# Performance work log

Hardware: AMD Instinct MI355X
Metric: run time of the kernel (lower is better)

Reference implementation:

```python
import jax, jax.numpy as jnp
import numpy as np

B, S = 64, 1024
D_INPUT, D_POLAR, N_LAYERS, KAN, N_CLASSES = 256, 256, 8, 32, 1000
PI = float(np.pi)
EPS = 1e-8


def _gelu(v):
    return jax.nn.gelu(v, approximate=False)  # torch nn.GELU default = exact erf


def setup_inputs() -> dict:
    key = jax.random.key(0)
    ks = jax.random.split(key, 16)

    def rn(k, shape, fan_in):
        return jax.random.normal(k, shape, jnp.float32) / np.sqrt(fan_in)

    return {
        "x": jax.random.normal(ks[0], (B, S, D_INPUT), jnp.float32),
        "embed_w": rn(ks[1], (D_INPUT, 2 * D_POLAR), D_INPUT),
        "embed_b": jnp.zeros((2 * D_POLAR,), jnp.float32),
        "mag_w1": rn(ks[2], (N_LAYERS, 1, KAN), 1),
        "mag_b1": jnp.zeros((N_LAYERS, KAN), jnp.float32),
        "mag_w2": rn(ks[3], (N_LAYERS, KAN, 1), KAN),
        "mag_b2": jnp.zeros((N_LAYERS, 1), jnp.float32),
        "ph_w1": rn(ks[4], (N_LAYERS, 2, KAN), 2),
        "ph_b1": jnp.zeros((N_LAYERS, KAN), jnp.float32),
        "ph_w2": rn(ks[5], (N_LAYERS, KAN, 2), KAN),
        "ph_b2": jnp.zeros((N_LAYERS, 2), jnp.float32),
        "cls_w1": rn(ks[6], (D_POLAR, KAN), D_POLAR),
        "cls_b1": jnp.zeros((KAN,), jnp.float32),
        "cls_w2": rn(ks[7], (KAN, N_CLASSES), KAN),
        "cls_b2": jnp.zeros((N_CLASSES,), jnp.float32),
    }


def _forward(x, embed_w, embed_b, mag_w1, mag_b1, mag_w2, mag_b2,
             ph_w1, ph_b1, ph_w2, ph_b2, cls_w1, cls_b1, cls_w2, cls_b2):
    h = x @ embed_w + embed_b                      # [B,S,2D]
    r = jnp.abs(h[..., :D_POLAR]) + 0.1            # [B,S,D]
    theta = h[..., D_POLAR:] * PI                  # [B,S,D]
    for i in range(N_LAYERS):
        xc = r * jnp.cos(theta)
        yc = r * jnp.sin(theta)
        xm = xc.mean(axis=1, keepdims=True)        # [B,1,D]
        ym = yc.mean(axis=1, keepdims=True)
        r_agg = jnp.sqrt(xm * xm + ym * ym + EPS)
        th_agg = jnp.arctan2(ym, xm)
        # magnitude MLP (1 -> 32 -> 1) in log space, per channel
        log_r = jnp.log(r_agg + EPS)[..., None]    # [B,1,D,1]
        lr = _gelu(log_r @ mag_w1[i] + mag_b1[i]) @ mag_w2[i] + mag_b2[i]
        r_trans = jnp.exp(lr[..., 0])              # [B,1,D]
        # phase MLP (2 -> 32 -> 2) on (sin, cos)
        pin = jnp.stack([jnp.sin(th_agg), jnp.cos(th_agg)], axis=-1)  # [B,1,D,2]
        pout = _gelu(pin @ ph_w1[i] + ph_b1[i]) @ ph_w2[i] + ph_b2[i]
        norm = jnp.sqrt(pout[..., 0] ** 2 + pout[..., 1] ** 2 + EPS)
        th_trans = jnp.arctan2(pout[..., 0] / norm, pout[..., 1] / norm)
        x_out = xc + r_trans * jnp.cos(th_trans)
        y_out = yc + r_trans * jnp.sin(th_trans)
        r = jnp.sqrt(x_out * x_out + y_out * y_out + EPS)
        theta = jnp.arctan2(y_out, x_out)
    pooled = r.mean(axis=1)                        # [B,D]
    return _gelu(pooled @ cls_w1 + cls_b1) @ cls_w2 + cls_b2  # [B,n_classes]


def reference(x, embed_w, embed_b, mag_w1, mag_b1, mag_w2, mag_b2,
              ph_w1, ph_b1, ph_w2, ph_b2, cls_w1, cls_b1, cls_w2, cls_b2):
    return _forward(x, embed_w, embed_b, mag_w1, mag_b1, mag_w2, mag_b2,
                    ph_w1, ph_b1, ph_w2, ph_b2, cls_w1, cls_b1, cls_w2, cls_b2)
```

## Files before the change

### kernel.cpp

```cpp
#include <hip/hip_runtime.h>
#include <hip/hip_bf16.h>
#include <hip/hip_fp16.h>

#define EPS 1e-8f
#define PI_F 3.14159265358979323846f

typedef _Float16 half8 __attribute__((ext_vector_type(8)));
typedef _Float16 half4 __attribute__((ext_vector_type(4)));
typedef float f32x4 __attribute__((ext_vector_type(4)));
typedef float f32x2 __attribute__((ext_vector_type(2)));

__device__ __forceinline__ float gelu_exact(float v) {
    return 0.5f * v * (1.0f + erff(v * 0.70710678118654752f));
}

__global__ void convertW(const float* __restrict__ W,
                         _Float16* __restrict__ Wth, _Float16* __restrict__ Wtl,
                         float* __restrict__ zero_base) {
    int idx = blockIdx.x * 256 + threadIdx.x;
    if (idx < 49152) zero_base[idx] = 0.f;
    int col = idx & 511, k = idx >> 9;
    int d = col & 255, g = d >> 6;
    int j = g * 128 + ((col < 256) ? (d & 63) : (64 + (d & 63)));
    float f = W[k * 512 + col];
    _Float16 h = (_Float16)f;
    Wth[j * 256 + k] = h;
    Wtl[j * 256 + k] = (_Float16)(f - (float)h);
}

__global__ __launch_bounds__(256, 4) void gemm_embed(
    const float* __restrict__ x,
    const _Float16* __restrict__ Wth, const _Float16* __restrict__ Wtl,
    const float* __restrict__ bias,
    unsigned short* __restrict__ XY8,
    float* __restrict__ XMsum, float* __restrict__ YMsum)
{
    __shared__ __attribute__((aligned(16))) _Float16 Ah[4096], Al[4096], Bh[4096], Bl[4096];
    const int tid  = threadIdx.x;
    const int wave = tid >> 6;
    const int lane = tid & 63;
    const int id   = blockIdx.x;
    const int xcd  = id & 7;
    const int s    = id >> 3;
    const int g    = s & 3;
    const int mt   = (s >> 2) * 8 + xcd;
    const int m0   = mt * 128;
    const int q    = lane >> 4, ln = lane & 15;

    f32x4 acc[8][2];
#pragma unroll
    for (int mi = 0; mi < 8; ++mi) {
        acc[mi][0] = (f32x4){0.f, 0.f, 0.f, 0.f};
        acc[mi][1] = (f32x4){0.f, 0.f, 0.f, 0.f};
    }

    for (int kt = 0; kt < 8; ++kt) {
        __syncthreads();
#pragma unroll
        for (int c2 = 0; c2 < 2; ++c2) {
            int idx = c2 * 256 + tid;
            int r = idx >> 2, c = idx & 3;
            size_t go = (size_t)(g * 128 + r) * 256 + kt * 32 + c * 8;
            half8 vh = *(const half8*)(Wth + go);
            half8 vl = *(const half8*)(Wtl + go);
            int pos = c ^ ((r >> 1) & 3);
            *(half8*)&Bh[r * 32 + pos * 8] = vh;
            *(half8*)&Bl[r * 32 + pos * 8] = vl;
        }
#pragma unroll
        for (int L = 0; L < 2; ++L) {
            int idx = L * 256 + tid;
            int r = idx >> 2, cq = idx & 3;
            const float* src = x + (size_t)(m0 + r) * 256 + kt * 32 + cq * 8;
            const float4 f0 = *(const float4*)(src);
            const float4 f1 = *(const float4*)(src + 4);
            half8 hh, ll;
            hh[0] = (_Float16)f0.x; ll[0] = (_Float16)(f0.x - (float)hh[0]);
            hh[1] = (_Float16)f0.y; ll[1] = (_Float16)(f0.y - (float)hh[1]);
            hh[2] = (_Float16)f0.z; ll[2] = (_Float16)(f0.z - (float)hh[2]);
            hh[3] = (_Float16)f0.w; ll[3] = (_Float16)(f0.w - (float)hh[3]);
            hh[4] = (_Float16)f1.x; ll[4] = (_Float16)(f1.x - (float)hh[4]);
            hh[5] = (_Float16)f1.y; ll[5] = (_Float16)(f1.y - (float)hh[5]);
            hh[6] = (_Float16)f1.z; ll[6] = (_Float16)(f1.z - (float)hh[6]);
            hh[7] = (_Float16)f1.w; ll[7] = (_Float16)(f1.w - (float)hh[7]);
            int pos = cq ^ ((r >> 1) & 3);
            *(half8*)&Ah[r * 32 + pos * 8] = hh;
            *(half8*)&Al[r * 32 + pos * 8] = ll;
        }
        __syncthreads();

        half8 bh[2], bl[2], am[8];
#pragma unroll
        for (int t = 0; t < 2; ++t) {
            int rn = (t * 4 + wave) * 16 + ln;
            int off = rn * 32 + (q ^ ((rn >> 1) & 3)) * 8;
            bh[t] = *(const half8*)&Bh[off];
            bl[t] = *(const half8*)&Bl[off];
        }
#pragma unroll
        for (int mi = 0; mi < 8; ++mi) {
            int row = mi * 16 + ln;
            am[mi] = *(const half8*)&Ah[row * 32 + (q ^ ((row >> 1) & 3)) * 8];
        }
#pragma unroll
        for (int mi = 0; mi < 8; ++mi)
#pragma unroll
            for (int t = 0; t < 2; ++t)
                acc[mi][t] = __builtin_amdgcn_mfma_f32_16x16x32_f16(am[mi], bh[t], acc[mi][t], 0, 0, 0);
#pragma unroll
        for (int mi = 0; mi < 8; ++mi)
#pragma unroll
            for (int t = 0; t < 2; ++t)
                acc[mi][t] = __builtin_amdgcn_mfma_f32_16x16x32_f16(am[mi], bl[t], acc[mi][t], 0, 0, 0);
#pragma unroll
        for (int mi = 0; mi < 8; ++mi) {
            int row = mi * 16 + ln;
            half8 alv = *(const half8*)&Al[row * 32 + (q ^ ((row >> 1) & 3)) * 8];
#pragma unroll
            for (int t = 0; t < 2; ++t)
                acc[mi][t] = __builtin_amdgcn_mfma_f32_16x16x32_f16(alv, bh[t], acc[mi][t], 0, 0, 0);
        }
    }

    const int d  = g * 64 + wave * 16 + ln;
    const int b  = m0 >> 10;
    const float b1 = bias[d];
    const float b2 = bias[256 + d];
    float sx = 0.f, sy = 0.f;
#pragma unroll
    for (int mi = 0; mi < 8; ++mi) {
#pragma unroll
        for (int i = 0; i < 4; ++i) {
            const int row = m0 + mi * 16 + q * 4 + i;
            const float h1 = acc[mi][0][i] + b1;
            const float h2 = acc[mi][1][i] + b2;
            const float rr = fabsf(h1) + 0.1f;
            float sv, cv;
            __sincosf(PI_F * h2, &sv, &cv);
            const float xc = rr * cv, yc = rr * sv;
            int pk = __builtin_amdgcn_cvt_pk_fp8_f32(xc, yc, 0, false);
            XY8[(size_t)row * 256 + d] = (unsigned short)pk;
            sx += xc; sy += yc;
        }
    }
    sx += __shfl_down(sx, 32); sx += __shfl_down(sx, 16);
    sy += __shfl_down(sy, 32); sy += __shfl_down(sy, 16);
    if (lane < 16) {
        atomicAdd(&XMsum[b * 256 + d], sx);
        atomicAdd(&YMsum[b * 256 + d], sy);
    }
}

__global__ __launch_bounds__(256) void layers_kernel(
    const float* __restrict__ XMsum, const float* __restrict__ YMsum,
    const float* __restrict__ mw1, const float* __restrict__ mb1,
    const float* __restrict__ mw2, const float* __restrict__ mb2,
    const float* __restrict__ pw1, const float* __restrict__ pb1,
    const float* __restrict__ pw2, const float* __restrict__ pb2,
    float* __restrict__ DX, float* __restrict__ DY)
{
    __shared__ float s_mw1[256], s_mb1[256], s_mw2[256], s_mb2[8];
    __shared__ float s_pw1[512], s_pb1[256], s_pw2[512], s_pb2[16];
    const int tid = threadIdx.x;
    s_mw1[tid] = mw1[tid]; s_mb1[tid] = mb1[tid];
    s_mw2[tid] = mw2[tid]; s_pb1[tid] = pb1[tid];
    s_pw1[tid] = pw1[tid]; s_pw1[256 + tid] = pw1[256 + tid];
    s_pw2[tid] = pw2[tid]; s_pw2[256 + tid] = pw2[256 + tid];
    if (tid < 8)  s_mb2[tid] = mb2[tid];
    if (tid < 16) s_pb2[tid] = pb2[tid];
    __syncthreads();

    const int gid = blockIdx.x * 256 + tid;
    const int idx = gid >> 3;
    const int sub = gid & 7;
    float xm = XMsum[idx] * (1.0f / 1024.0f);
    float ym = YMsum[idx] * (1.0f / 1024.0f);
    float dxa = 0.f, dya = 0.f;
#pragma unroll 1
    for (int i = 0; i < 8; ++i) {
        float r2    = xm * xm + ym * ym;
        float r_agg = sqrtf(r2 + EPS);
        float hyp   = sqrtf(r2);
        float inv   = hyp > 0.f ? 1.0f / hyp : 0.f;
        float st    = ym * inv;
        float ct    = hyp > 0.f ? xm * inv : 1.0f;
        float log_r = logf(r_agg + EPS);
        float lr = 0.f, p0 = 0.f, p1 = 0.f;
#pragma unroll
        for (int k4 = 0; k4 < 4; ++k4) {
            int k = sub * 4 + k4;
            float hm = gelu_exact(log_r * s_mw1[i * 32 + k] + s_mb1[i * 32 + k]);
            lr += hm * s_mw2[i * 32 + k];
            float hp = gelu_exact(st * s_pw1[i * 64 + k] + ct * s_pw1[i * 64 + 32 + k] + s_pb1[i * 32 + k]);
            p0 += hp * s_pw2[i * 64 + 2 * k + 0];
            p1 += hp * s_pw2[i * 64 + 2 * k + 1];
        }
        lr += __shfl_xor(lr, 1); lr += __shfl_xor(lr, 2); lr += __shfl_xor(lr, 4);
        p0 += __shfl_xor(p0, 1); p0 += __shfl_xor(p0, 2); p0 += __shfl_xor(p0, 4);
        p1 += __shfl_xor(p1, 1); p1 += __shfl_xor(p1, 2); p1 += __shfl_xor(p1, 4);
        lr += s_mb2[i];
        p0 += s_pb2[i * 2 + 0];
        p1 += s_pb2[i * 2 + 1];
        float r_trans = expf(lr);
        float hp2  = sqrtf(p0 * p0 + p1 * p1);
        float invp = hp2 > 0.f ? 1.0f / hp2 : 0.f;
        float ctt  = hp2 > 0.f ? p1 * invp : 1.0f;
        float stt  = p0 * invp;
        float dx = r_trans * ctt;
        float dy = r_trans * stt;
        dxa += dx; dya += dy; xm += dx; ym += dy;
    }
    if (sub == 0) { DX[idx] = dxa; DY[idx] = dya; }
}

__global__ __launch_bounds__(256) void pool_kernel(
    const unsigned short* __restrict__ XY8,
    const float* __restrict__ DX, const float* __restrict__ DY,
    float* __restrict__ pooled)
{
    __shared__ float red[256][9];
    const int b = blockIdx.x, sc = blockIdx.y, tid = threadIdx.x;
    const int dg = tid & 31;
    const int sh = tid >> 5;
    const int d0 = dg * 8;
    float dxv[8], dyv[8], s[8];
#pragma unroll
    for (int j = 0; j < 8; ++j) {
        dxv[j] = DX[b * 256 + d0 + j];
        dyv[j] = DY[b * 256 + d0 + j];
        s[j] = 0.f;
    }
    const int r0 = sc * 128 + sh * 16;
    const size_t base = ((size_t)b * 1024 + r0) * 256 + d0;
#pragma unroll 4
    for (int i = 0; i < 16; ++i) {
        const int4 v = *(const int4*)(XY8 + base + (size_t)i * 256);
        const int wv[4] = {v.x, v.y, v.z, v.w};
#pragma unroll
        for (int w = 0; w < 4; ++w) {
            f32x2 pa = __builtin_amdgcn_cvt_pk_f32_fp8(wv[w], false);
            f32x2 pb = __builtin_amdgcn_cvt_pk_f32_fp8(wv[w], true);
            float xa = pa[0] + dxv[2 * w],     ya = pa[1] + dyv[2 * w];
            float xb = pb[0] + dxv[2 * w + 1], yb = pb[1] + dyv[2 * w + 1];
            s[2 * w]     += sqrtf(xa * xa + ya * ya + EPS);
            s[2 * w + 1] += sqrtf(xb * xb + yb * yb + EPS);
        }
    }
#pragma unroll
    for (int j = 0; j < 8; ++j) red[tid][j] = s[j];
    __syncthreads();
    if (tid < 32) {
#pragma unroll
        for (int j = 0; j < 8; ++j) {
            float t = 0.f;
#pragma unroll
            for (int c = 0; c < 8; ++c) t += red[c * 32 + tid][j];
            atomicAdd(&pooled[b * 256 + tid * 8 + j], t);
        }
    }
}

__global__ __launch_bounds__(256) void cls_kernel(
    const float* __restrict__ pooled,
    const float* __restrict__ w1, const float* __restrict__ b1,
    const float* __restrict__ w2, const float* __restrict__ b2,
    float* __restrict__ out)
{
    __shared__ float pl[256];
    __shared__ float part[8][32];
    __shared__ float hd[32];
    const int b = blockIdx.x, tid = threadIdx.x;
    pl[tid] = pooled[b * 256 + tid] * (1.0f / 1024.0f);
    __syncthreads();
    const int hu = tid & 31, kc = tid >> 5;
    float a = 0.f;
    for (int k = kc * 32; k < kc * 32 + 32; ++k) a += pl[k] * w1[k * 32 + hu];
    part[kc][hu] = a;
    __syncthreads();
    if (tid < 32) {
        float s = b1[tid];
#pragma unroll
        for (int c = 0; c < 8; ++c) s += part[c][tid];
        hd[tid] = gelu_exact(s);
    }
    __syncthreads();
    for (int n = tid; n < 1000; n += 256) {
        float s = b2[n];
#pragma unroll
        for (int k = 0; k < 32; ++k) s += hd[k] * w2[k * 1000 + n];
        out[b * 1000 + n] = s;
    }
}

extern "C" void kernel_launch(void* const* d_in, const int* in_sizes, int n_in,
                              void* d_out, int out_size, void* d_ws, size_t ws_size,
                              hipStream_t stream)
{
    const float* x       = (const float*)d_in[0];
    const float* embed_w = (const float*)d_in[1];
    const float* embed_b = (const float*)d_in[2];
    const float* mag_w1  = (const float*)d_in[3];
    const float* mag_b1  = (const float*)d_in[4];
    const float* mag_w2  = (const float*)d_in[5];
    const float* mag_b2  = (const float*)d_in[6];
    const float* ph_w1   = (const float*)d_in[7];
    const float* ph_b1   = (const float*)d_in[8];
    const float* ph_w2   = (const float*)d_in[9];
    const float* ph_b2   = (const float*)d_in[10];
    const float* cls_w1  = (const float*)d_in[11];
    const float* cls_b1  = (const float*)d_in[12];
    const float* cls_w2  = (const float*)d_in[13];
    const float* cls_b2  = (const float*)d_in[14];
    float* out = (float*)d_out;

    char* ws = (char*)d_ws;
    unsigned short* XY8 = (unsigned short*)(ws + 0);
    _Float16* Wth = (_Float16*)(ws + 33554432);
    _Float16* Wtl = (_Float16*)(ws + 33816576);
    float* XMsum  = (float*)(ws + 34078720);
    float* YMsum  = (float*)(ws + 34144256);
    float* pooled = (float*)(ws + 34209792);
    float* DX     = (float*)(ws + 34275328);
    float* DY     = (float*)(ws + 34340864);

    convertW<<<512, 256, 0, stream>>>(embed_w, Wth, Wtl, XMsum);
    gemm_embed<<<2048, 256, 0, stream>>>(x, Wth, Wtl, embed_b, XY8, XMsum, YMsum);
    layers_kernel<<<512, 256, 0, stream>>>(XMsum, YMsum, mag_w1, mag_b1, mag_w2, mag_b2,
                                           ph_w1, ph_b1, ph_w2, ph_b2, DX, DY);
    pool_kernel<<<dim3(64, 8), 256, 0, stream>>>(XY8, DX, DY, pooled);
    cls_kernel<<<64, 256, 0, stream>>>(pooled, cls_w1, cls_b1, cls_w2, cls_b2, out);
}
```

Before: 213.1 us.

## Load GEMM fragments directly from global memory, dropping LDS staging in embed GEMM

The embed GEMM no longer stages A and B tiles through shared memory with barriers. Each wave now loads its own MFMA fragments straight from global memory, converting x to split fp16 hi/lo in registers. The wave layout changes from 128x16 per wave to a 2x2 arrangement of 64x32 tiles, and occupancy is lowered to 2 blocks via launch bounds. This removes LDS traffic and synchronisation, but x rows are re-read and re-converted by two waves and loads become less coalesced, relying on cache hits.

```diff
diff --git a/kernel.cpp b/kernel.cpp
--- a/kernel.cpp
+++ b/kernel.cpp
@@ -6,7 +6,6 @@
 #define PI_F 3.14159265358979323846f
 
 typedef _Float16 half8 __attribute__((ext_vector_type(8)));
-typedef _Float16 half4 __attribute__((ext_vector_type(4)));
 typedef float f32x4 __attribute__((ext_vector_type(4)));
 typedef float f32x2 __attribute__((ext_vector_type(2)));
 
@@ -28,52 +27,58 @@
     Wtl[j * 256 + k] = (_Float16)(f - (float)h);
 }
 
-__global__ __launch_bounds__(256, 4) void gemm_embed(
+__global__ __launch_bounds__(256, 2) void gemm_embed(
     const float* __restrict__ x,
     const _Float16* __restrict__ Wth, const _Float16* __restrict__ Wtl,
     const float* __restrict__ bias,
     unsigned short* __restrict__ XY8,
     float* __restrict__ XMsum, float* __restrict__ YMsum)
 {
-    __shared__ __attribute__((aligned(16))) _Float16 Ah[4096], Al[4096], Bh[4096], Bl[4096];
     const int tid  = threadIdx.x;
     const int wave = tid >> 6;
     const int lane = tid & 63;
     const int id   = blockIdx.x;
     const int xcd  = id & 7;
-    const int s    = id >> 3;
-    const int g    = s & 3;
-    const int mt   = (s >> 2) * 8 + xcd;
+    const int sidx = id >> 3;
+    const int g    = sidx & 3;
+    const int mt   = (sidx >> 2) * 8 + xcd;
     const int m0   = mt * 128;
     const int q    = lane >> 4, ln = lane & 15;
-
-    f32x4 acc[8][2];
-#pragma unroll
-    for (int mi = 0; mi < 8; ++mi) {
-        acc[mi][0] = (f32x4){0.f, 0.f, 0.f, 0.f};
-        acc[mi][1] = (f32x4){0.f, 0.f, 0.f, 0.f};
-    }
-
+    const int mh   = wave & 1;
+    const int a2   = wave >> 1;
+
+    int offA[4];
+#pragma unroll
+    for (int mi = 0; mi < 4; ++mi)
+        offA[mi] = (m0 + mh * 64 + mi * 16 + ln) * 256 + q * 8;
+
+    int offB[4];
+#pragma unroll
+    for (int t = 0; t < 4; ++t) {
+        int grp = 2 * a2 + (t & 1) + ((t >> 1) << 2);
+        offB[t] = (g * 128 + grp * 16 + ln) * 256 + q * 8;
+    }
+
+    f32x4 acc[4][4];
+#pragma unroll
+    for (int mi = 0; mi < 4; ++mi)
+#pragma unroll
+        for (int t = 0; t < 4; ++t)
+            acc[mi][t] = (f32x4){0.f, 0.f, 0.f, 0.f};
+
+#pragma unroll 2
     for (int kt = 0; kt < 8; ++kt) {
-        __syncthreads();
-#pragma unroll
-        for (int c2 = 0; c2 < 2; ++c2) {
-            int idx = c2 * 256 + tid;
-            int r = idx >> 2, c = idx & 3;
-            size_t go = (size_t)(g * 128 + r) * 256 + kt * 32 + c * 8;
-            half8 vh = *(const half8*)(Wth + go);
-            half8 vl = *(const half8*)(Wtl + go);
-            int pos = c ^ ((r >> 1) & 3);
-            *(half8*)&Bh[r * 32 + pos * 8] = vh;
-            *(half8*)&Bl[r * 32 + pos * 8] = vl;
-        }
-#pragma unroll
-        for (int L = 0; L < 2; ++L) {
-            int idx = L * 256 + tid;
-            int r = idx >> 2, cq = idx & 3;
-            const float* src = x + (size_t)(m0 + r) * 256 + kt * 32 + cq * 8;
-            const float4 f0 = *(const float4*)(src);
-            const float4 f1 = *(const float4*)(src + 4);
+        const int ka = kt * 32;
+        half8 bh[4], bl[4], ah[4], al[4];
+#pragma unroll
+        for (int t = 0; t < 4; ++t) {
+            bh[t] = *(const half8*)(Wth + (offB[t] + ka));
+            bl[t] = *(const half8*)(Wtl + (offB[t] + ka));
+        }
+#pragma unroll
+        for (int mi = 0; mi < 4; ++mi) {
+            const float4 f0 = *(const float4*)(x + (offA[mi] + ka));
+            const float4 f1 = *(const float4*)(x + (offA[mi] + ka + 4));
             half8 hh, ll;
             hh[0] = (_Float16)f0.x; ll[0] = (_Float16)(f0.x - (float)hh[0]);
             hh[1] = (_Float16)f0.y; ll[1] = (_Float16)(f0.y - (float)hh[1]);
@@ -83,71 +88,54 @@
             hh[5] = (_Float16)f1.y; ll[5] = (_Float16)(f1.y - (float)hh[5]);
             hh[6] = (_Float16)f1.z; ll[6] = (_Float16)(f1.z - (float)hh[6]);
             hh[7] = (_Float16)f1.w; ll[7] = (_Float16)(f1.w - (float)hh[7]);
-            int pos = cq ^ ((r >> 1) & 3);
-            *(half8*)&Ah[r * 32 + pos * 8] = hh;
-            *(half8*)&Al[r * 32 + pos * 8] = ll;
-        }
-        __syncthreads();
-
-        half8 bh[2], bl[2], am[8];
-#pragma unroll
-        for (int t = 0; t < 2; ++t) {
-            int rn = (t * 4 + wave) * 16 + ln;
-            int off = rn * 32 + (q ^ ((rn >> 1) & 3)) * 8;
-            bh[t] = *(const half8*)&Bh[off];
-            bl[t] = *(const half8*)&Bl[off];
-        }
-#pragma unroll
-        for (int mi = 0; mi < 8; ++mi) {
-            int row = mi * 16 + ln;
-            am[mi] = *(const half8*)&Ah[row * 32 + (q ^ ((row >> 1) & 3)) * 8];
-        }
-#pragma unroll
-        for (int mi = 0; mi < 8; ++mi)
-#pragma unroll
-            for (int t = 0; t < 2; ++t)
-                acc[mi][t] = __builtin_amdgcn_mfma_f32_16x16x32_f16(am[mi], bh[t], acc[mi][t], 0, 0, 0);
-#pragma unroll
-        for (int mi = 0; mi < 8; ++mi)
-#pragma unroll
-            for (int t = 0; t < 2; ++t)
-                acc[mi][t] = __builtin_amdgcn_mfma_f32_16x16x32_f16(am[mi], bl[t], acc[mi][t], 0, 0, 0);
-#pragma unroll
-        for (int mi = 0; mi < 8; ++mi) {
-            int row = mi * 16 + ln;
-            half8 alv = *(const half8*)&Al[row * 32 + (q ^ ((row >> 1) & 3)) * 8];
-#pragma unroll
-            for (int t = 0; t < 2; ++t)
-                acc[mi][t] = __builtin_amdgcn_mfma_f32_16x16x32_f16(alv, bh[t], acc[mi][t], 0, 0, 0);
-        }
-    }
-
-    const int d  = g * 64 + wave * 16 + ln;
-    const int b  = m0 >> 10;
-    const float b1 = bias[d];
-    const float b2 = bias[256 + d];
-    float sx = 0.f, sy = 0.f;
-#pragma unroll
-    for (int mi = 0; mi < 8; ++mi) {
-#pragma unroll
-        for (int i = 0; i < 4; ++i) {
-            const int row = m0 + mi * 16 + q * 4 + i;
-            const float h1 = acc[mi][0][i] + b1;
-            const float h2 = acc[mi][1][i] + b2;
-            const float rr = fabsf(h1) + 0.1f;
-            float sv, cv;
-            __sincosf(PI_F * h2, &sv, &cv);
-            const float xc = rr * cv, yc = rr * sv;
-            int pk = __builtin_amdgcn_cvt_pk_fp8_f32(xc, yc, 0, false);
-            XY8[(size_t)row * 256 + d] = (unsigned short)pk;
-            sx += xc; sy += yc;
-        }
-    }
-    sx += __shfl_down(sx, 32); sx += __shfl_down(sx, 16);
-    sy += __shfl_down(sy, 32); sy += __shfl_down(sy, 16);
-    if (lane < 16) {
-        atomicAdd(&XMsum[b * 256 + d], sx);
-        atomicAdd(&YMsum[b * 256 + d], sy);
+            ah[mi] = hh; al[mi] = ll;
+        }
+#pragma unroll
+        for (int mi = 0; mi < 4; ++mi)
+#pragma unroll
+            for (int t = 0; t < 4; ++t)
+                acc[mi][t] = __builtin_amdgcn_mfma_f32_16x16x32_f16(ah[mi], bh[t], acc[mi][t], 0, 0, 0);
+#pragma unroll
+        for (int mi = 0; mi < 4; ++mi)
+#pragma unroll
+            for (int t = 0; t < 4; ++t)
+                acc[mi][t] = __builtin_amdgcn_mfma_f32_16x16x32_f16(ah[mi], bl[t], acc[mi][t], 0, 0, 0);
+#pragma unroll
+        for (int mi = 0; mi < 4; ++mi)
+#pragma unroll
+            for (int t = 0; t < 4; ++t)
+                acc[mi][t] = __builtin_amdgcn_mfma_f32_16x16x32_f16(al[mi], bh[t], acc[mi][t], 0, 0, 0);
+    }
+
+    const int b = m0 >> 10;
+#pragma unroll
+    for (int t01 = 0; t01 < 2; ++t01) {
+        const int d  = g * 64 + (2 * a2 + t01) * 16 + ln;
+        const float b1 = bias[d];
+        const float b2 = bias[256 + d];
+        float sx = 0.f, sy = 0.f;
+#pragma unroll
+        for (int mi = 0; mi < 4; ++mi) {
+#pragma unroll
+            for (int i = 0; i < 4; ++i) {
+                const int row = m0 + mh * 64 + mi * 16 + q * 4 + i;
+                const float h1 = acc[mi][t01][i] + b1;
+                const float h2 = acc[mi][t01 + 2][i] + b2;
+                const float rr = fabsf(h1) + 0.1f;
+                float sv, cv;
+                __sincosf(PI_F * h2, &sv, &cv);
+                const float xc = rr * cv, yc = rr * sv;
+                int pk = __builtin_amdgcn_cvt_pk_fp8_f32(xc, yc, 0, false);
+                XY8[(size_t)row * 256 + d] = (unsigned short)pk;
+                sx += xc; sy += yc;
+            }
+        }
+        sx += __shfl_down(sx, 32); sx += __shfl_down(sx, 16);
+        sy += __shfl_down(sy, 32); sy += __shfl_down(sy, 16);
+        if (lane < 16) {
+            atomicAdd(&XMsum[b * 256 + d], sx);
+            atomicAdd(&YMsum[b * 256 + d], sy);
+        }
     }
 }
 
```

After: 268.7 us. 26.1% more time.

## Fuse layer MLP, pooling and classifier into one tail kernel

Applied to the files above, without the earlier changes.

Replaces the separate layers, pool and classifier kernels with a single kernel where each block recomputes the per-batch layer offsets into shared memory, pools its row chunk, and the last block per batch (via an atomic counter) runs the classifier. This removes two launches and the DX/DY global round trip. It adds redundant layer MLP compute per block (8x replicated, serial over 32 hidden units) and a counter that must be zeroed each call.

```diff
diff --git a/kernel.cpp b/kernel.cpp
--- a/kernel.cpp
+++ b/kernel.cpp
@@ -6,7 +6,6 @@
 #define PI_F 3.14159265358979323846f
 
 typedef _Float16 half8 __attribute__((ext_vector_type(8)));
-typedef _Float16 half4 __attribute__((ext_vector_type(4)));
 typedef float f32x4 __attribute__((ext_vector_type(4)));
 typedef float f32x2 __attribute__((ext_vector_type(2)));
 
@@ -18,7 +17,7 @@
                          _Float16* __restrict__ Wth, _Float16* __restrict__ Wtl,
                          float* __restrict__ zero_base) {
     int idx = blockIdx.x * 256 + threadIdx.x;
-    if (idx < 49152) zero_base[idx] = 0.f;
+    if (idx < 49216) zero_base[idx] = 0.f;
     int col = idx & 511, k = idx >> 9;
     int d = col & 255, g = d >> 6;
     int j = g * 128 + ((col < 256) ? (d & 63) : (64 + (d & 63)));
@@ -151,17 +150,28 @@
     }
 }
 
-__global__ __launch_bounds__(256) void layers_kernel(
+__global__ __launch_bounds__(256) void tail_kernel(
+    const unsigned short* __restrict__ XY8,
     const float* __restrict__ XMsum, const float* __restrict__ YMsum,
     const float* __restrict__ mw1, const float* __restrict__ mb1,
     const float* __restrict__ mw2, const float* __restrict__ mb2,
     const float* __restrict__ pw1, const float* __restrict__ pb1,
     const float* __restrict__ pw2, const float* __restrict__ pb2,
-    float* __restrict__ DX, float* __restrict__ DY)
+    const float* __restrict__ cw1, const float* __restrict__ cb1,
+    const float* __restrict__ cw2, const float* __restrict__ cb2,
+    float* __restrict__ pooled, unsigned* __restrict__ cnt,
+    float* __restrict__ out)
 {
     __shared__ float s_mw1[256], s_mb1[256], s_mw2[256], s_mb2[8];
     __shared__ float s_pw1[512], s_pb1[256], s_pw2[512], s_pb2[16];
+    __shared__ float sdx[256], sdy[256];
+    __shared__ float red[256][9];
+    __shared__ float pl[256], part[8][32], hd[32];
+    __shared__ int last_flag;
     const int tid = threadIdx.x;
+    const int bid = blockIdx.x;
+    const int b = bid >> 3, sc = bid & 7;
+
     s_mw1[tid] = mw1[tid]; s_mb1[tid] = mb1[tid];
     s_mw2[tid] = mw2[tid]; s_pb1[tid] = pb1[tid];
     s_pw1[tid] = pw1[tid]; s_pw1[256 + tid] = pw1[256 + tid];
@@ -170,125 +180,115 @@
     if (tid < 16) s_pb2[tid] = pb2[tid];
     __syncthreads();
 
-    const int gid = blockIdx.x * 256 + tid;
-    const int idx = gid >> 3;
-    const int sub = gid & 7;
-    float xm = XMsum[idx] * (1.0f / 1024.0f);
-    float ym = YMsum[idx] * (1.0f / 1024.0f);
-    float dxa = 0.f, dya = 0.f;
+    {
+        const int idx = b * 256 + tid;
+        float xm = XMsum[idx] * (1.0f / 1024.0f);
+        float ym = YMsum[idx] * (1.0f / 1024.0f);
+        float dxa = 0.f, dya = 0.f;
 #pragma unroll 1
-    for (int i = 0; i < 8; ++i) {
-        float r2    = xm * xm + ym * ym;
-        float r_agg = sqrtf(r2 + EPS);
-        float hyp   = sqrtf(r2);
-        float inv   = hyp > 0.f ? 1.0f / hyp : 0.f;
-        float st    = ym * inv;
-        float ct    = hyp > 0.f ? xm * inv : 1.0f;
-        float log_r = logf(r_agg + EPS);
-        float lr = 0.f, p0 = 0.f, p1 = 0.f;
-#pragma unroll
-        for (int k4 = 0; k4 < 4; ++k4) {
-            int k = sub * 4 + k4;
-            float hm = gelu_exact(log_r * s_mw1[i * 32 + k] + s_mb1[i * 32 + k]);
-            lr += hm * s_mw2[i * 32 + k];
-            float hp = gelu_exact(st * s_pw1[i * 64 + k] + ct * s_pw1[i * 64 + 32 + k] + s_pb1[i * 32 + k]);
-            p0 += hp * s_pw2[i * 64 + 2 * k + 0];
-            p1 += hp * s_pw2[i * 64 + 2 * k + 1];
-        }
-        lr += __shfl_xor(lr, 1); lr += __shfl_xor(lr, 2); lr += __shfl_xor(lr, 4);
-        p0 += __shfl_xor(p0, 1); p0 += __shfl_xor(p0, 2); p0 += __shfl_xor(p0, 4);
-        p1 += __shfl_xor(p1, 1); p1 += __shfl_xor(p1, 2); p1 += __shfl_xor(p1, 4);
-        lr += s_mb2[i];
-        p0 += s_pb2[i * 2 + 0];
-        p1 += s_pb2[i * 2 + 1];
-        float r_trans = expf(lr);
-        float hp2  = sqrtf(p0 * p0 + p1 * p1);
-        float invp = hp2 > 0.f ? 1.0f / hp2 : 0.f;
-        float ctt  = hp2 > 0.f ? p1 * invp : 1.0f;
-        float stt  = p0 * invp;
-        float dx = r_trans * ctt;
-        float dy = r_trans * stt;
-        dxa += dx; dya += dy; xm += dx; ym += dy;
-    }
-    if (sub == 0) { DX[idx] = dxa; DY[idx] = dya; }
-}
-
-__global__ __launch_bounds__(256) void pool_kernel(
-    const unsigned short* __restrict__ XY8,
-    const float* __restrict__ DX, const float* __restrict__ DY,
-    float* __restrict__ pooled)
-{
-    __shared__ float red[256][9];
-    const int b = blockIdx.x, sc = blockIdx.y, tid = threadIdx.x;
-    const int dg = tid & 31;
-    const int sh = tid >> 5;
-    const int d0 = dg * 8;
-    float dxv[8], dyv[8], s[8];
-#pragma unroll
-    for (int j = 0; j < 8; ++j) {
-        dxv[j] = DX[b * 256 + d0 + j];
-        dyv[j] = DY[b * 256 + d0 + j];
-        s[j] = 0.f;
-    }
-    const int r0 = sc * 128 + sh * 16;
-    const size_t base = ((size_t)b * 1024 + r0) * 256 + d0;
+        for (int i = 0; i < 8; ++i) {
+            float r2    = xm * xm + ym * ym;
+            float r_agg = sqrtf(r2 + EPS);
+            float hyp   = sqrtf(r2);
+            float inv   = hyp > 0.f ? 1.0f / hyp : 0.f;
+            float st    = ym * inv;
+            float ct    = hyp > 0.f ? xm * inv : 1.0f;
+            float log_r = logf(r_agg + EPS);
+            float lr = s_mb2[i];
+            float p0 = s_pb2[i * 2 + 0], p1 = s_pb2[i * 2 + 1];
 #pragma unroll 4
-    for (int i = 0; i < 16; ++i) {
-        const int4 v = *(const int4*)(XY8 + base + (size_t)i * 256);
-        const int wv[4] = {v.x, v.y, v.z, v.w};
-#pragma unroll
-        for (int w = 0; w < 4; ++w) {
-            f32x2 pa = __builtin_amdgcn_cvt_pk_f32_fp8(wv[w], false);
-            f32x2 pb = __builtin_amdgcn_cvt_pk_f32_fp8(wv[w], true);
-            float xa = pa[0] + dxv[2 * w],     ya = pa[1] + dyv[2 * w];
-            float xb = pb[0] + dxv[2 * w + 1], yb = pb[1] + dyv[2 * w + 1];
-            s[2 * w]     += sqrtf(xa * xa + ya * ya + EPS);
-            s[2 * w + 1] += sqrtf(xb * xb + yb * yb + EPS);
-        }
-    }
-#pragma unroll
-    for (int j = 0; j < 8; ++j) red[tid][j] = s[j];
-    __syncthreads();
-    if (tid < 32) {
+            for (int k = 0; k < 32; ++k) {
+                float hm = gelu_exact(log_r * s_mw1[i * 32 + k] + s_mb1[i * 32 + k]);
+                lr += hm * s_mw2[i * 32 + k];
+                float hp = gelu_exact(st * s_pw1[i * 64 + k] + ct * s_pw1[i * 64 + 32 + k] + s_pb1[i * 32 + k]);
+                p0 += hp * s_pw2[i * 64 + 2 * k + 0];
+                p1 += hp * s_pw2[i * 64 + 2 * k + 1];
+            }
+            float r_trans = expf(lr);
+            float hp2  = sqrtf(p0 * p0 + p1 * p1);
+            float invp = hp2 > 0.f ? 1.0f / hp2 : 0.f;
+            float ctt  = hp2 > 0.f ? p1 * invp : 1.0f;
+            float stt  = p0 * invp;
+            float dx = r_trans * ctt;
+            float dy = r_trans * stt;
+            dxa += dx; dya += dy; xm += dx; ym += dy;
+        }
+        sdx[tid] = dxa; sdy[tid] = dya;
+    }
+    __syncthreads();
+
+    {
+        const int dg = tid & 31;
+        const int sh = tid >> 5;
+        const int d0 = dg * 8;
+        float dxv[8], dyv[8], sacc[8];
 #pragma unroll
         for (int j = 0; j < 8; ++j) {
-            float t = 0.f;
-#pragma unroll
-            for (int c = 0; c < 8; ++c) t += red[c * 32 + tid][j];
-            atomicAdd(&pooled[b * 256 + tid * 8 + j], t);
-        }
-    }
-}
-
-__global__ __launch_bounds__(256) void cls_kernel(
-    const float* __restrict__ pooled,
-    const float* __restrict__ w1, const float* __restrict__ b1,
-    const float* __restrict__ w2, const float* __restrict__ b2,
-    float* __restrict__ out)
-{
-    __shared__ float pl[256];
-    __shared__ float part[8][32];
-    __shared__ float hd[32];
-    const int b = blockIdx.x, tid = threadIdx.x;
-    pl[tid] = pooled[b * 256 + tid] * (1.0f / 1024.0f);
+            dxv[j] = sdx[d0 + j];
+            dyv[j] = sdy[d0 + j];
+            sacc[j] = 0.f;
+        }
+        const int r0 = sc * 128 + sh * 16;
+        const size_t base = ((size_t)b * 1024 + r0) * 256 + d0;
+#pragma unroll 4
+        for (int i = 0; i < 16; ++i) {
+            const int4 v = *(const int4*)(XY8 + base + (size_t)i * 256);
+            const int wv[4] = {v.x, v.y, v.z, v.w};
+#pragma unroll
+            for (int w = 0; w < 4; ++w) {
+                f32x2 pa = __builtin_amdgcn_cvt_pk_f32_fp8(wv[w], false);
+                f32x2 pb = __builtin_amdgcn_cvt_pk_f32_fp8(wv[w], true);
+                float xa = pa[0] + dxv[2 * w],     ya = pa[1] + dyv[2 * w];
+                float xb = pb[0] + dxv[2 * w + 1], yb = pb[1] + dyv[2 * w + 1];
+                sacc[2 * w]     += sqrtf(xa * xa + ya * ya + EPS);
+                sacc[2 * w + 1] += sqrtf(xb * xb + yb * yb + EPS);
+            }
+        }
+#pragma unroll
+        for (int j = 0; j < 8; ++j) red[tid][j] = sacc[j];
+        __syncthreads();
+        if (tid < 32) {
+#pragma unroll
+            for (int j = 0; j < 8; ++j) {
+                float t = 0.f;
+#pragma unroll
+                for (int c = 0; c < 8; ++c) t += red[c * 32 + tid][j];
+                atomicAdd(&pooled[b * 256 + tid * 8 + j], t);
+            }
+        }
+    }
+    __syncthreads();
+
+    if (tid == 0) {
+        __threadfence();
+        unsigned old = __hip_atomic_fetch_add(&cnt[b], 1u, __ATOMIC_ACQ_REL,
+                                              __HIP_MEMORY_SCOPE_AGENT);
+        last_flag = (old == 7u);
+    }
+    __syncthreads();
+    if (!last_flag) return;
+    __threadfence();
+
+    pl[tid] = __hip_atomic_load(&pooled[b * 256 + tid], __ATOMIC_RELAXED,
+                                __HIP_MEMORY_SCOPE_AGENT) * (1.0f / 1024.0f);
     __syncthreads();
     const int hu = tid & 31, kc = tid >> 5;
     float a = 0.f;
-    for (int k = kc * 32; k < kc * 32 + 32; ++k) a += pl[k] * w1[k * 32 + hu];
+    for (int k = kc * 32; k < kc * 32 + 32; ++k) a += pl[k] * cw1[k * 32 + hu];
     part[kc][hu] = a;
     __syncthreads();
     if (tid < 32) {
-        float s = b1[tid];
-#pragma unroll
-        for (int c = 0; c < 8; ++c) s += part[c][tid];
-        hd[tid] = gelu_exact(s);
+        float s2 = cb1[tid];
+#pragma unroll
+        for (int c = 0; c < 8; ++c) s2 += part[c][tid];
+        hd[tid] = gelu_exact(s2);
     }
     __syncthreads();
     for (int n = tid; n < 1000; n += 256) {
-        float s = b2[n];
-#pragma unroll
-        for (int k = 0; k < 32; ++k) s += hd[k] * w2[k * 1000 + n];
-        out[b * 1000 + n] = s;
+        float s2 = cb2[n];
+#pragma unroll
+        for (int k = 0; k < 32; ++k) s2 += hd[k] * cw2[k * 1000 + n];
+        out[b * 1000 + n] = s2;
     }
 }
 
@@ -320,13 +320,13 @@
     float* XMsum  = (float*)(ws + 34078720);
     float* YMsum  = (float*)(ws + 34144256);
     float* pooled = (float*)(ws + 34209792);
-    float* DX     = (float*)(ws + 34275328);
-    float* DY     = (float*)(ws + 34340864);
+    unsigned* cnt = (unsigned*)(ws + 34275328);
 
     convertW<<<512, 256, 0, stream>>>(embed_w, Wth, Wtl, XMsum);
     gemm_embed<<<2048, 256, 0, stream>>>(x, Wth, Wtl, embed_b, XY8, XMsum, YMsum);
-    layers_kernel<<<512, 256, 0, stream>>>(XMsum, YMsum, mag_w1, mag_b1, mag_w2, mag_b2,
-                                           ph_w1, ph_b1, ph_w2, ph_b2, DX, DY);
-    pool_kernel<<<dim3(64, 8), 256, 0, stream>>>(XY8, DX, DY, pooled);
-    cls_kernel<<<64, 256, 0, stream>>>(pooled, cls_w1, cls_b1, cls_w2, cls_b2, out);
-}
+    tail_kernel<<<512, 256, 0, stream>>>(XY8, XMsum, YMsum,
+                                         mag_w1, mag_b1, mag_w2, mag_b2,
+                                         ph_w1, ph_b1, ph_w2, ph_b2,
+                                         cls_w1, cls_b1, cls_w2, cls_b2,
+                                         pooled, cnt, out);
+}
```

After: 279.5 us. 1.31x slower.
